# Kernel optimization log

Measured on AMD Instinct MI355X. Metric: run time of the kernel, lower is better.

Reference implementation:

```python
import jax, jax.numpy as jnp
import numpy as np
from functools import partial

B = 8192
BS = 6           # board_size
NSQ = BS * BS    # 36
FLAT = 128 * NSQ # 4608
EPS = 1e-5


def _conv(x, w, b):
    # x: (N,C,H,W), w: (O,I,3,3), SAME padding
    y = jax.lax.conv_general_dilated(x, w, (1, 1), 'SAME',
                                     dimension_numbers=('NCHW', 'OIHW', 'NCHW'))
    return y + b[None, :, None, None]


def _bn_eval(x, g, b, m, v):
    inv = jax.lax.rsqrt(v + EPS)
    return (x - m[None, :, None, None]) * (g * inv)[None, :, None, None] + b[None, :, None, None]


def _ln(x, g, b):
    mu = jnp.mean(x, axis=-1, keepdims=True)
    var = jnp.mean(jnp.square(x - mu), axis=-1, keepdims=True)
    return (x - mu) * jax.lax.rsqrt(var + EPS) * g + b


def _lin(x, w, b):
    return x @ w.T + b


def setup_inputs() -> dict:
    key = jax.random.key(0)
    ks = iter(jax.random.split(key, 64))
    nrm = lambda shape, s=0.05: jax.random.normal(next(ks), shape, jnp.float32) * s
    d = {}
    d['x'] = jax.random.normal(next(ks), (B, 4, BS, BS), jnp.float32)
    d['conv1_w'] = nrm((64, 4, 3, 3)); d['conv1_b'] = nrm((64,))
    d['bn1_g'] = jnp.ones((64,)); d['bn1_b'] = jnp.zeros((64,))
    d['bn1_m'] = nrm((64,)); d['bn1_v'] = jnp.ones((64,))
    d['conv2_w'] = nrm((128, 64, 3, 3)); d['conv2_b'] = nrm((128,))
    d['bn2_g'] = jnp.ones((128,)); d['bn2_b'] = jnp.zeros((128,))
    d['bn2_m'] = nrm((128,)); d['bn2_v'] = jnp.ones((128,))
    d['conv3_w'] = nrm((128, 128, 3, 3)); d['conv3_b'] = nrm((128,))
    d['bn3_g'] = jnp.ones((128,)); d['bn3_b'] = jnp.zeros((128,))
    d['bn3_m'] = nrm((128,)); d['bn3_v'] = jnp.ones((128,))
    d['pfc1_w'] = nrm((256, FLAT)); d['pfc1_b'] = nrm((256,))
    d['pln_g'] = jnp.ones((256,)); d['pln_b'] = jnp.zeros((256,))
    d['pfc2_w'] = nrm((NSQ, 256)); d['pfc2_b'] = nrm((NSQ,))
    d['mfc1_w'] = nrm((256, FLAT + NSQ)); d['mfc1_b'] = nrm((256,))
    d['mln_g'] = jnp.ones((256,)); d['mln_b'] = jnp.zeros((256,))
    d['mfc2_w'] = nrm((NSQ, 256)); d['mfc2_b'] = nrm((NSQ,))
    d['vfc1_w'] = nrm((256, FLAT)); d['vfc1_b'] = nrm((256,))
    d['vln_g'] = jnp.ones((256,)); d['vln_b'] = jnp.zeros((256,))
    d['vfc2_w'] = nrm((1, 256)); d['vfc2_b'] = nrm((1,))
    return d


def reference(x, conv1_w, conv1_b, bn1_g, bn1_b, bn1_m, bn1_v,
              conv2_w, conv2_b, bn2_g, bn2_b, bn2_m, bn2_v,
              conv3_w, conv3_b, bn3_g, bn3_b, bn3_m, bn3_v,
              pfc1_w, pfc1_b, pln_g, pln_b, pfc2_w, pfc2_b,
              mfc1_w, mfc1_b, mln_g, mln_b, mfc2_w, mfc2_b,
              vfc1_w, vfc1_b, vln_g, vln_b, vfc2_w, vfc2_b):
    h = jax.nn.relu(_bn_eval(_conv(x, conv1_w, conv1_b), bn1_g, bn1_b, bn1_m, bn1_v))
    h = jax.nn.relu(_bn_eval(_conv(h, conv2_w, conv2_b), bn2_g, bn2_b, bn2_m, bn2_v))
    h = jax.nn.relu(_bn_eval(_conv(h, conv3_w, conv3_b), bn3_g, bn3_b, bn3_m, bn3_v))
    feats = h.reshape(-1, FLAT)  # (B, 4608)

    piece_h = jax.nn.relu(_ln(_lin(feats, pfc1_w, pfc1_b), pln_g, pln_b))
    piece_logits = _lin(piece_h, pfc2_w, pfc2_b)  # (B, 36)

    # eval-mode: one-hot of argmax piece
    sel = jax.nn.one_hot(jnp.argmax(piece_logits, axis=1), NSQ, dtype=feats.dtype)
    move_in = jnp.concatenate([feats, sel], axis=1)  # (B, 4644)
    move_h = jax.nn.relu(_ln(_lin(move_in, mfc1_w, mfc1_b), mln_g, mln_b))
    move_logits = _lin(move_h, mfc2_w, mfc2_b)  # (B, 36)

    val_h = jax.nn.relu(_ln(_lin(feats, vfc1_w, vfc1_b), vln_g, vln_b))
    val = _lin(val_h, vfc2_w, vfc2_b)  # (B, 1)

    piece_adv = piece_logits - jnp.mean(piece_logits, axis=1, keepdims=True)
    move_adv = move_logits - jnp.mean(move_logits, axis=1, keepdims=True)

    # action_idx = i*36 + j  ->  fused outer-sum broadcast, reshape to (B, 1296)
    q = val[:, :, None] + piece_adv[:, :, None] + move_adv[:, None, :]
    return q.reshape(-1, NSQ * NSQ)
```

## Files before the change

kernel.cpp:

```cpp
#include <hip/hip_runtime.h>
#include <hip/hip_bf16.h>

#define BQ 8192
#define CHUNK 2048
#define NCHUNK 4
typedef __attribute__((ext_vector_type(8))) __bf16 bf16x8;
typedef __attribute__((ext_vector_type(4))) float f32x4;
typedef __attribute__((ext_vector_type(4))) int int4v;

__device__ __forceinline__ f32x4 mfma16(bf16x8 a, bf16x8 b, f32x4 c) {
    return __builtin_amdgcn_mfma_f32_16x16x32_bf16(a, b, c, 0, 0, 0);
}

__device__ __forceinline__ void split3(float v, __hip_bfloat16& s0,
                                       __hip_bfloat16& s1, __hip_bfloat16& s2) {
    s0 = __float2bfloat16(v);
    float r = v - __bfloat162float(s0);
    s1 = __float2bfloat16(r);
    r -= __bfloat162float(s1);
    s2 = __float2bfloat16(r);
}

__device__ __forceinline__ int pair_a(int pp) { return (0x211000 >> (4 * pp)) & 0xF; }
__device__ __forceinline__ int pair_w(int pp) { return (0x010210 >> (4 * pp)) & 0xF; }


__global__ void prep_scalars_k(
    const float* __restrict__ c1b, const float* __restrict__ g1,
    const float* __restrict__ b1,  const float* __restrict__ m1,
    const float* __restrict__ v1,
    const float* __restrict__ c2b, const float* __restrict__ g2,
    const float* __restrict__ b2,  const float* __restrict__ m2,
    const float* __restrict__ v2,
    const float* __restrict__ c3b, const float* __restrict__ g3,
    const float* __restrict__ b3,  const float* __restrict__ m3,
    const float* __restrict__ v3,
    const float* __restrict__ pfb, const float* __restrict__ vfb,
    const float* __restrict__ mfb,
    float* __restrict__ scale1, float* __restrict__ bias1f,
    float* __restrict__ scale2, float* __restrict__ bias2f,
    float* __restrict__ scale3, float* __restrict__ bias3f,
    float* __restrict__ biasfc)
{
    int t = threadIdx.x;
    if (t < 64) {
        float s = g1[t] * rsqrtf(v1[t] + 1e-5f);
        scale1[t] = s;
        bias1f[t] = (c1b[t] - m1[t]) * s + b1[t];
    }
    if (t < 128) {
        float s2 = g2[t] * rsqrtf(v2[t] + 1e-5f);
        scale2[t] = s2;
        bias2f[t] = (c2b[t] - m2[t]) * s2 + b2[t];
        float s3 = g3[t] * rsqrtf(v3[t] + 1e-5f);
        scale3[t] = s3;
        bias3f[t] = (c3b[t] - m3[t]) * s3 + b3[t];
    }
    if (t < 256)      biasfc[t] = pfb[t];
    else if (t < 512) biasfc[t] = vfb[t - 256];
    else              biasfc[t] = mfb[t - 512];
}

template<int CIN>
__global__ void prep_convw_k(const float* __restrict__ w,
                             __hip_bfloat16* __restrict__ wt, size_t planeW)
{
    int id = blockIdx.x * 256 + threadIdx.x;
    int kk = id & 31;
    int n  = (id >> 5) & 127;
    int kt = id >> 12;
    int k  = kt * 32 + kk;
    int s  = k / CIN;
    int i  = k & (CIN - 1);
    __hip_bfloat16 s0, s1, s2;
    split3(w[(n * CIN + i) * 9 + s], s0, s1, s2);
    size_t dest = (size_t)kt * 4096 + ((n >> 5) * 1024) + (((n >> 4) & 1) * 512)
                + ((kk >> 3) * 128) + ((n & 15) * 8) + (kk & 7);
    wt[dest] = s0; wt[dest + planeW] = s1; wt[dest + 2 * planeW] = s2;
}

__global__ void prep_bigw_k(const float* __restrict__ pw,
                            const float* __restrict__ vw,
                            const float* __restrict__ mw,
                            __hip_bfloat16* __restrict__ bigw, size_t planeBW)
{
    int id = blockIdx.x * 256 + threadIdx.x;
    int kk = id & 31;
    int n  = (id >> 5) % 768;
    int kt = id / (32 * 768);
    int k2 = kt * 32 + kk;
    int c  = k2 & 127, p = k2 >> 7;
    int k  = c * 36 + p;
    float v;
    if (n < 256)      v = pw[n * 4608 + k];
    else if (n < 512) v = vw[(n - 256) * 4608 + k];
    else              v = mw[(n - 512) * 4644 + k];
    __hip_bfloat16 s0, s1, s2;
    split3(v, s0, s1, s2);
    size_t dest = (size_t)kt * 24576 + ((n >> 7) * 4096) + (((n >> 6) & 1) * 2048)
                + (((n >> 4) & 3) * 512) + ((kk >> 3) * 128) + ((n & 15) * 8) + (kk & 7);
    bigw[dest] = s0; bigw[dest + planeBW] = s1; bigw[dest + 2 * planeBW] = s2;
}

__global__ void prep_selw_k(const float* __restrict__ mw,
                            float* __restrict__ selw)
{
    int j = blockIdx.x, d = threadIdx.x;
    selw[j * 256 + d] = mw[d * 4644 + 4608 + j];
}


__global__ __launch_bounds__(256)
void conv1_k(const float* __restrict__ x,
             const float* __restrict__ w,
             const float* __restrict__ scale, const float* __restrict__ biasf,
             __hip_bfloat16* __restrict__ out, size_t planeA,
             int b_base)
{
    __shared__ float wl[64 * 37];
    int tid = threadIdx.x;
    for (int c = tid; c < 64 * 36; c += 256) {
        int o = c / 36, k = c - o * 36;
        wl[o * 37 + k] = w[c];
    }
    __syncthreads();
    unsigned gid = blockIdx.x * 256 + tid;
    int o = gid & 63;
    unsigned bp = gid >> 6;
    unsigned b = bp / 36;
    int p = bp - b * 36;
    int py = p / 6, px = p - py * 6;
    const float* xb = x + (size_t)(b_base + b) * 4 * 36;
    float acc = 0.f;
#pragma unroll
    for (int i = 0; i < 4; ++i) {
#pragma unroll
        for (int s = 0; s < 9; ++s) {
            int ny = py + s / 3 - 1, nx = px + s % 3 - 1;
            if ((unsigned)ny < 6u && (unsigned)nx < 6u)
                acc += xb[i * 36 + ny * 6 + nx] * wl[o * 37 + i * 9 + s];
        }
    }
    float v = fmaxf(acc * scale[o] + biasf[o], 0.f);
    __hip_bfloat16 s0, s1, s2;
    split3(v, s0, s1, s2);
    size_t idx = (size_t)bp * 64 + o;
    out[idx] = s0; out[idx + planeA] = s1; out[idx + 2 * planeA] = s2;
}

template<int CIN>
__global__ __launch_bounds__(256, 4)
void conv_gemm_k(const __hip_bfloat16* __restrict__ in, size_t planeA,
                 const __hip_bfloat16* __restrict__ wt, size_t planeW,
                 const float* __restrict__ scale,
                 const float* __restrict__ biasf,
                 __hip_bfloat16* __restrict__ out, size_t planeO)
{
    constexpr int PS  = CIN + 8;
    constexpr int CPB = CIN / 32;
    constexpr int NSLICE = CPB * 9;
    constexpr int XS_ELEMS = 72 * PS;
    __shared__ __align__(16) __hip_bfloat16 smem[XS_ELEMS + CIN];
    __hip_bfloat16* xs = smem;

    const int tid  = threadIdx.x;
    const int wave = tid >> 6, lane = tid & 63;
    const int m16  = lane & 15, quad = lane >> 4;
    const int b0   = blockIdx.x * 2;

    if (tid < CIN) smem[XS_ELEMS + tid] = __float2bfloat16(0.f);

    f32x4 acc[5][2];
#pragma unroll
    for (int i = 0; i < 5; ++i) { acc[i][0] = f32x4{0,0,0,0}; acc[i][1] = f32x4{0,0,0,0}; }

    const int bo0 = wave * 1024 + lane * 8;
    const int bo1 = bo0 + 512;

    constexpr int CHPP = CIN / 8;
    for (int pp = 0; pp < 6; ++pp) {
        const __hip_bfloat16* inb = in + (size_t)pair_a(pp) * planeA + (size_t)b0 * 36 * CIN;
        const __hip_bfloat16* wP  = wt + (size_t)pair_w(pp) * planeW;
        const bool stage_x = (pp == 0) || (pair_a(pp) != pair_a(pp - 1));

        if (stage_x) {
            __syncthreads();
            for (int c = tid; c < 72 * CHPP; c += 256) {
                int pix = c / CHPP;
                int off = (c - pix * CHPP) * 8;
                *(int4v*)(xs + pix * PS + off) = *(const int4v*)(inb + pix * CIN + off);
            }
            __syncthreads();
        }

        bf16x8 wc0 = *(const bf16x8*)(wP + bo0);
        bf16x8 wc1 = *(const bf16x8*)(wP + bo1);

        for (int s = 0; s < 9; ++s) {
            const int dy = s / 3 - 1, dx = s % 3 - 1;
            int aoff[5];
#pragma unroll
            for (int rt = 0; rt < 5; ++rt) {
                int m   = rt * 16 + m16;
                int img = m >= 36;
                int p   = m - img * 36;
                int py  = p / 6, px = p - py * 6;
                int ny  = py + dy, nx = px + dx;
                bool ok = (m < 72) && ((unsigned)ny < 6u) && ((unsigned)nx < 6u);
                int base = ok ? ((img * 36 + ny * 6 + nx) * PS) : XS_ELEMS;
                aoff[rt] = base + quad * 8;
            }
#pragma unroll
            for (int c = 0; c < CPB; ++c) {
                const int kt = s * CPB + c;
                const int ktn = (kt + 1 < NSLICE) ? (kt + 1) : 0;
                const __hip_bfloat16* wN = wP + (size_t)ktn * 4096;
                bf16x8 wn0 = *(const bf16x8*)(wN + bo0);
                bf16x8 wn1 = *(const bf16x8*)(wN + bo1);
                const int coff = c * 32;
#pragma unroll
                for (int rt = 0; rt < 5; ++rt) {
                    bf16x8 af = *(const bf16x8*)(smem + aoff[rt] + coff);
                    acc[rt][0] = mfma16(af, wc0, acc[rt][0]);
                    acc[rt][1] = mfma16(af, wc1, acc[rt][1]);
                }
                wc0 = wn0; wc1 = wn1;
            }
        }
    }

#pragma unroll
    for (int ct = 0; ct < 2; ++ct) {
        const int n = wave * 32 + ct * 16 + m16;
        const float sc = scale[n], bi = biasf[n];
#pragma unroll
        for (int rt = 0; rt < 5; ++rt) {
            const int mrow = rt * 16 + quad * 4;
            if (mrow < 72) {
#pragma unroll
                for (int r = 0; r < 4; ++r) {
                    float v = fmaxf(acc[rt][ct][r] * sc + bi, 0.f);
                    __hip_bfloat16 s0, s1, s2;
                    split3(v, s0, s1, s2);
                    size_t idx = (size_t)(b0 * 36 + mrow + r) * 128 + n;
                    out[idx] = s0; out[idx + planeO] = s1; out[idx + 2 * planeO] = s2;
                }
            }
        }
    }
}


template<int NW, int NKT>
__device__ __forceinline__ void fc_body(
    const __hip_bfloat16* __restrict__ Ap,
    const __hip_bfloat16* __restrict__ Bp,
    size_t planeBW, int kt0,
    float* __restrict__ outp, size_t m0,
    __hip_bfloat16* smem, int tid, int wave, int lane)
{
    constexpr int ABUF = 4096;
    constexpr int NPH = NW * NKT;
    const int m16 = lane & 15, quad = lane >> 4;
    const int wr = wave >> 1, wc = wave & 1;
    const int cr = tid >> 2, co = (tid & 3) * 8;

    f32x4 acc[4][4];
#pragma unroll
    for (int i = 0; i < 4; ++i)
#pragma unroll
        for (int j = 0; j < 4; ++j) acc[i][j] = f32x4{0,0,0,0};

    int ao[4];
#pragma unroll
    for (int i = 0; i < 4; ++i) ao[i] = wr * 2048 + i * 512 + lane * 8;
    const int bofs = wc * 2048 + lane * 8;
    const int adst = ((cr >> 4) & 3) * 512 + (tid & 3) * 128 + (cr & 15) * 8;

    auto ldA = [&](int ktr, int4v& a0, int4v& a1) {
        const __hip_bfloat16* base = Ap + (m0 + cr) * 4608 + (kt0 + ktr) * 32 + co;
        a0 = *(const int4v*)base;
        a1 = *(const int4v*)(base + (size_t)64 * 4608);
    };
    auto ldB = [&](int p, bf16x8* bf) {
        const int ktr = p / NW, w = p - ktr * NW;
        const __hip_bfloat16* base = Bp + (size_t)w * planeBW
                                   + (size_t)(kt0 + ktr) * 24576 + bofs;
#pragma unroll
        for (int i = 0; i < 4; ++i) bf[i] = *(const bf16x8*)(base + i * 512);
    };
    auto stA = [&](int buf, int4v a0, int4v a1) {
        __hip_bfloat16* base = smem + buf * ABUF;
        *(int4v*)(base + adst) = a0;
        *(int4v*)(base + 2048 + adst) = a1;
    };

    int4v pa0, pa1, qa0, qa1;
    bf16x8 Bc[4], B1[4], Bn[4];
    {
        int4v a0, a1;
        ldA(0, a0, a1);
        ldB(0, Bc);
        ldA(1, pa0, pa1);
        if (NPH > 1) ldB(1, B1);
        stA(0, a0, a1);
    }
    __syncthreads();
    int cur = 0;

    for (int ktr = 0; ktr < NKT; ++ktr) {
        { int ktn = (ktr + 2 < NKT) ? (ktr + 2) : 0; ldA(ktn, qa0, qa1); }
        const __hip_bfloat16* base = smem + cur * ABUF;
        bf16x8 af[4];
#pragma unroll
        for (int i = 0; i < 4; ++i) af[i] = *(const bf16x8*)(base + ao[i]);
#pragma unroll
        for (int w = 0; w < NW; ++w) {
            int p2 = ktr * NW + w + 2;
            if (p2 >= NPH) p2 = 0;
            ldB(p2, Bn);
#pragma unroll
            for (int i = 0; i < 4; ++i)
#pragma unroll
                for (int j = 0; j < 4; ++j)
                    acc[i][j] = mfma16(af[i], Bc[j], acc[i][j]);
#pragma unroll
            for (int i = 0; i < 4; ++i) { Bc[i] = B1[i]; B1[i] = Bn[i]; }
        }
        if (ktr + 1 < NKT) stA(cur ^ 1, pa0, pa1);
        __syncthreads();
        cur ^= 1;
        pa0 = qa0; pa1 = qa1;
    }

#pragma unroll
    for (int i = 0; i < 4; ++i) {
        const int row = wr * 64 + i * 16 + quad * 4;
#pragma unroll
        for (int j = 0; j < 4; ++j) {
            const int col = wc * 64 + j * 16 + m16;
#pragma unroll
            for (int r = 0; r < 4; ++r)
                outp[(m0 + row + r) * 768 + col] = acc[i][j][r];
        }
    }
}

__global__ __launch_bounds__(256, 3)
void fc_partial_k(const __hip_bfloat16* __restrict__ A, size_t planeF,
                  const __hip_bfloat16* __restrict__ Bw, size_t planeBW,
                  float* __restrict__ partial)
{
    constexpr int ABUF = 4096;
    __shared__ __align__(16) __hip_bfloat16 smem[2 * ABUF];
    const int tid = threadIdx.x, wave = tid >> 6, lane = tid & 63;
    const int mblk = blockIdx.x & 15;
    int rest = blockIdx.x >> 4;
    const int nblk = rest % 6;
    const int slot = rest / 6;
    const size_t m0 = (size_t)mblk * 128;

    const __hip_bfloat16* Bp = Bw + (size_t)nblk * 4096;
    float* outp = partial + (size_t)slot * CHUNK * 768 + (size_t)nblk * 128;

    if (slot < 6) {
        fc_body<3, 24>(A, Bp, planeBW, slot * 24, outp, m0, smem, tid, wave, lane);
    } else if (slot < 10) {
        fc_body<2, 36>(A + planeF, Bp, planeBW, (slot - 6) * 36, outp, m0, smem, tid, wave, lane);
    } else {
        fc_body<1, 72>(A + 2 * planeF, Bp, planeBW, (slot - 10) * 72, outp, m0, smem, tid, wave, lane);
    }
}


__global__ __launch_bounds__(256)
void heads_k(const float* __restrict__ partial,
             const float* __restrict__ biasfc,
             const float* __restrict__ pln_g, const float* __restrict__ pln_b,
             const float* __restrict__ pfc2_w, const float* __restrict__ pfc2_b,
             const float* __restrict__ mln_g, const float* __restrict__ mln_b,
             const float* __restrict__ mfc2_w, const float* __restrict__ mfc2_b,
             const float* __restrict__ vln_g, const float* __restrict__ vln_b,
             const float* __restrict__ vfc2_w, const float* __restrict__ vfc2_b,
             const float* __restrict__ selw,
             float* __restrict__ q,
             int b_base)
{
    __shared__ float hp[256], hv[256], hm[256];
    __shared__ float pl[36], ml[36];
    __shared__ float red[4];
    __shared__ float valv, plm_s, mlm_s;
    __shared__ int amax_s;

    const int tid = threadIdx.x, wave = tid >> 6, lane = tid & 63;
    const size_t b = blockIdx.x;
    const size_t bg = b_base + b;

    float pp = biasfc[tid], vv = biasfc[256 + tid], mm = biasfc[512 + tid];
#pragma unroll
    for (int k = 0; k < 12; ++k) {
        const float* row = partial + (size_t)k * CHUNK * 768 + b * 768;
        pp += row[tid]; vv += row[256 + tid]; mm += row[512 + tid];
    }

    auto warpSum = [&](float v) {
        v += __shfl_xor(v, 1);  v += __shfl_xor(v, 2);  v += __shfl_xor(v, 4);
        v += __shfl_xor(v, 8);  v += __shfl_xor(v, 16); v += __shfl_xor(v, 32);
        return v;
    };
    auto blockSum = [&](float v) {
        v = warpSum(v);
        if (lane == 0) red[wave] = v;
        __syncthreads();
        float s = red[0] + red[1] + red[2] + red[3];
        __syncthreads();
        return s;
    };
    auto lnrelu = [&](float x, const float* g, const float* bb) {
        float mu  = blockSum(x) * (1.f / 256.f);
        float d   = x - mu;
        float var = blockSum(d * d) * (1.f / 256.f);
        float y   = d * rsqrtf(var + 1e-5f) * g[tid] + bb[tid];
        return fmaxf(y, 0.f);
    };

    hp[tid] = lnrelu(pp, pln_g, pln_b);
    hv[tid] = lnrelu(vv, vln_g, vln_b);
    __syncthreads();

    {
        float h0 = hp[lane], h1 = hp[64 + lane], h2 = hp[128 + lane], h3 = hp[192 + lane];
#pragma unroll
        for (int jj = 0; jj < 9; ++jj) {
            int j = wave * 9 + jj;
            const float* wr_ = pfc2_w + j * 256;
            float s = h0 * wr_[lane] + h1 * wr_[64 + lane]
                    + h2 * wr_[128 + lane] + h3 * wr_[192 + lane];
            s = warpSum(s);
            if (lane == 0) pl[j] = s + pfc2_b[j];
        }
        if (wave == 0) {
            float g0 = hv[lane], g1 = hv[64 + lane], g2 = hv[128 + lane], g3 = hv[192 + lane];
            float s = g0 * vfc2_w[lane] + g1 * vfc2_w[64 + lane]
                    + g2 * vfc2_w[128 + lane] + g3 * vfc2_w[192 + lane];
            s = warpSum(s);
            if (lane == 0) valv = s + vfc2_b[0];
        }
    }
    __syncthreads();
    if (tid == 0) {
        float m = -1e30f, s = 0.f; int idx = 0;
        for (int j = 0; j < 36; ++j) { float v = pl[j]; s += v; if (v > m) { m = v; idx = j; } }
        plm_s = s * (1.f / 36.f); amax_s = idx;
    }
    __syncthreads();

    mm += selw[amax_s * 256 + tid];
    hm[tid] = lnrelu(mm, mln_g, mln_b);
    __syncthreads();
    {
        float h0 = hm[lane], h1 = hm[64 + lane], h2 = hm[128 + lane], h3 = hm[192 + lane];
#pragma unroll
        for (int jj = 0; jj < 9; ++jj) {
            int j = wave * 9 + jj;
            const float* wr_ = mfc2_w + j * 256;
            float s = h0 * wr_[lane] + h1 * wr_[64 + lane]
                    + h2 * wr_[128 + lane] + h3 * wr_[192 + lane];
            s = warpSum(s);
            if (lane == 0) ml[j] = s + mfc2_b[j];
        }
    }
    __syncthreads();
    if (tid == 0) {
        float s = 0.f;
        for (int j = 0; j < 36; ++j) s += ml[j];
        mlm_s = s * (1.f / 36.f);
    }
    __syncthreads();

    const float val = valv, plm = plm_s, mlm = mlm_s;
    for (int idx = tid; idx < 1296; idx += 256) {
        int i = idx / 36, j = idx - i * 36;
        q[bg * 1296 + idx] = val + (pl[i] - plm) + (ml[j] - mlm);
    }
}


extern "C" void kernel_launch(void* const* d_in, const int* in_sizes, int n_in,
                              void* d_out, int out_size, void* d_ws, size_t ws_size,
                              hipStream_t stream)
{
    const float* x       = (const float*)d_in[0];
    const float* conv1_w = (const float*)d_in[1];
    const float* conv1_b = (const float*)d_in[2];
    const float* bn1_g   = (const float*)d_in[3];
    const float* bn1_b   = (const float*)d_in[4];
    const float* bn1_m   = (const float*)d_in[5];
    const float* bn1_v   = (const float*)d_in[6];
    const float* conv2_w = (const float*)d_in[7];
    const float* conv2_b = (const float*)d_in[8];
    const float* bn2_g   = (const float*)d_in[9];
    const float* bn2_b   = (const float*)d_in[10];
    const float* bn2_m   = (const float*)d_in[11];
    const float* bn2_v   = (const float*)d_in[12];
    const float* conv3_w = (const float*)d_in[13];
    const float* conv3_b = (const float*)d_in[14];
    const float* bn3_g   = (const float*)d_in[15];
    const float* bn3_b   = (const float*)d_in[16];
    const float* bn3_m   = (const float*)d_in[17];
    const float* bn3_v   = (const float*)d_in[18];
    const float* pfc1_w  = (const float*)d_in[19];
    const float* pfc1_b  = (const float*)d_in[20];
    const float* pln_g   = (const float*)d_in[21];
    const float* pln_b   = (const float*)d_in[22];
    const float* pfc2_w  = (const float*)d_in[23];
    const float* pfc2_b  = (const float*)d_in[24];
    const float* mfc1_w  = (const float*)d_in[25];
    const float* mfc1_b  = (const float*)d_in[26];
    const float* mln_g   = (const float*)d_in[27];
    const float* mln_b   = (const float*)d_in[28];
    const float* mfc2_w  = (const float*)d_in[29];
    const float* mfc2_b  = (const float*)d_in[30];
    const float* vfc1_w  = (const float*)d_in[31];
    const float* vfc1_b  = (const float*)d_in[32];
    const float* vln_g   = (const float*)d_in[33];
    const float* vln_b   = (const float*)d_in[34];
    const float* vfc2_w  = (const float*)d_in[35];
    const float* vfc2_b  = (const float*)d_in[36];

    const size_t planeW2 = 576 * 128;
    const size_t planeW3 = 1152 * 128;
    const size_t planeBW = (size_t)4608 * 768;
    const size_t planeA1 = (size_t)CHUNK * 36 * 64;
    const size_t planeA2 = (size_t)CHUNK * 36 * 128;

    char* ws = (char*)d_ws;
    size_t off = 0;
    auto alloc = [&](size_t bytes) -> char* {
        char* p = ws + off; off += (bytes + 255) & ~(size_t)255; return p;
    };
    __hip_bfloat16* w2t  = (__hip_bfloat16*)alloc(3 * planeW2 * 2);
    __hip_bfloat16* w3t  = (__hip_bfloat16*)alloc(3 * planeW3 * 2);
    __hip_bfloat16* bigw = (__hip_bfloat16*)alloc(3 * planeBW * 2);
    float* selw   = (float*)alloc(36 * 256 * 4);
    float* scale1 = (float*)alloc(64 * 4);
    float* bias1f = (float*)alloc(64 * 4);
    float* scale2 = (float*)alloc(128 * 4);
    float* bias2f = (float*)alloc(128 * 4);
    float* scale3 = (float*)alloc(128 * 4);
    float* bias3f = (float*)alloc(128 * 4);
    float* biasfc = (float*)alloc(768 * 4);
    char* A1 = alloc(3 * planeA2 * 2);
    char* A2 = alloc((size_t)12 * CHUNK * 768 * 4);

    prep_scalars_k<<<1, 768, 0, stream>>>(
        conv1_b, bn1_g, bn1_b, bn1_m, bn1_v,
        conv2_b, bn2_g, bn2_b, bn2_m, bn2_v,
        conv3_b, bn3_g, bn3_b, bn3_m, bn3_v,
        pfc1_b, vfc1_b, mfc1_b,
        scale1, bias1f, scale2, bias2f, scale3, bias3f, biasfc);
    prep_convw_k<64><<<288, 256, 0, stream>>>(conv2_w, w2t, planeW2);
    prep_convw_k<128><<<576, 256, 0, stream>>>(conv3_w, w3t, planeW3);
    prep_bigw_k<<<13824, 256, 0, stream>>>(pfc1_w, vfc1_w, mfc1_w, bigw, planeBW);
    prep_selw_k<<<36, 256, 0, stream>>>(mfc1_w, selw);

    __hip_bfloat16* h1s  = (__hip_bfloat16*)A1;
    __hip_bfloat16* h2s  = (__hip_bfloat16*)A2;
    __hip_bfloat16* h3s  = (__hip_bfloat16*)A1;
    float*          fpar = (float*)A2;

    for (int cchunk = 0; cchunk < NCHUNK; ++cchunk) {
        const int b_base = cchunk * CHUNK;
        conv1_k<<<CHUNK * 36 * 64 / 256, 256, 0, stream>>>(
            x, conv1_w, scale1, bias1f, h1s, planeA1, b_base);
        conv_gemm_k<64><<<CHUNK / 2, 256, 0, stream>>>(
            h1s, planeA1, w2t, planeW2, scale2, bias2f, h2s, planeA2);
        conv_gemm_k<128><<<CHUNK / 2, 256, 0, stream>>>(
            h2s, planeA2, w3t, planeW3, scale3, bias3f, h3s, planeA2);
        fc_partial_k<<<1152, 256, 0, stream>>>(h3s, planeA2, bigw, planeBW, fpar);
        heads_k<<<CHUNK, 256, 0, stream>>>(fpar, biasfc,
            pln_g, pln_b, pfc2_w, pfc2_b,
            mln_g, mln_b, mfc2_w, mfc2_b,
            vln_g, vln_b, vfc2_w, vfc2_b,
            selw, (float*)d_out, b_base);
    }
}
```

Baseline: 1.698 ms.

## Use larger batch chunks with fewer split-K slots when workspace allows

When the workspace is large enough, the kernel processes the batch in chunks of 4096 instead of 2048 and splits the FC reduction into 6 slots instead of 12. Each FC block then runs a longer K loop, and the heads kernel sums fewer partials. This cuts launch count and partial-sum traffic. In exchange the FC loop trip count becomes a runtime value with unroll 2, which may cost some scheduling quality. The conv kernels also get more blocks per launch, and the path taken depends on ws_size at runtime.

```diff
diff --git a/kernel.cpp b/kernel.cpp
--- a/kernel.cpp
+++ b/kernel.cpp
@@ -2,8 +2,6 @@
 #include <hip/hip_bf16.h>
 
 #define BQ 8192
-#define CHUNK 2048
-#define NCHUNK 4
 typedef __attribute__((ext_vector_type(8))) __bf16 bf16x8;
 typedef __attribute__((ext_vector_type(4))) float f32x4;
 typedef __attribute__((ext_vector_type(4))) int int4v;
@@ -251,16 +249,16 @@
 }
 
 
-template<int NW, int NKT>
+template<int NW>
 __device__ __forceinline__ void fc_body(
     const __hip_bfloat16* __restrict__ Ap,
     const __hip_bfloat16* __restrict__ Bp,
-    size_t planeBW, int kt0,
+    size_t planeBW, int kt0, int NKT,
     float* __restrict__ outp, size_t m0,
     __hip_bfloat16* smem, int tid, int wave, int lane)
 {
     constexpr int ABUF = 4096;
-    constexpr int NPH = NW * NKT;
+    const int NPH = NW * NKT;
     const int m16 = lane & 15, quad = lane >> 4;
     const int wr = wave >> 1, wc = wave & 1;
     const int cr = tid >> 2, co = (tid & 3) * 8;
@@ -308,6 +306,7 @@
     __syncthreads();
     int cur = 0;
 
+#pragma unroll 2
     for (int ktr = 0; ktr < NKT; ++ktr) {
         { int ktn = (ktr + 2 < NKT) ? (ktr + 2) : 0; ldA(ktn, qa0, qa1); }
         const __hip_bfloat16* base = smem + cur * ABUF;
@@ -349,26 +348,36 @@
 __global__ __launch_bounds__(256, 3)
 void fc_partial_k(const __hip_bfloat16* __restrict__ A, size_t planeF,
                   const __hip_bfloat16* __restrict__ Bw, size_t planeBW,
-                  float* __restrict__ partial)
+                  float* __restrict__ partial,
+                  int chunk, int big)
 {
     constexpr int ABUF = 4096;
     __shared__ __align__(16) __hip_bfloat16 smem[2 * ABUF];
     const int tid = threadIdx.x, wave = tid >> 6, lane = tid & 63;
-    const int mblk = blockIdx.x & 15;
-    int rest = blockIdx.x >> 4;
+    const int nmblk = chunk >> 7;
+    const int mblk = blockIdx.x & (nmblk - 1);
+    int rest = blockIdx.x / nmblk;
     const int nblk = rest % 6;
     const int slot = rest / 6;
     const size_t m0 = (size_t)mblk * 128;
 
     const __hip_bfloat16* Bp = Bw + (size_t)nblk * 4096;
-    float* outp = partial + (size_t)slot * CHUNK * 768 + (size_t)nblk * 128;
-
-    if (slot < 6) {
-        fc_body<3, 24>(A, Bp, planeBW, slot * 24, outp, m0, smem, tid, wave, lane);
-    } else if (slot < 10) {
-        fc_body<2, 36>(A + planeF, Bp, planeBW, (slot - 6) * 36, outp, m0, smem, tid, wave, lane);
+    float* outp = partial + (size_t)slot * chunk * 768 + (size_t)nblk * 128;
+
+    if (big) {
+        if (slot < 3)
+            fc_body<3>(A, Bp, planeBW, slot * 48, 48, outp, m0, smem, tid, wave, lane);
+        else if (slot < 5)
+            fc_body<2>(A + planeF, Bp, planeBW, (slot - 3) * 72, 72, outp, m0, smem, tid, wave, lane);
+        else
+            fc_body<1>(A + 2 * planeF, Bp, planeBW, 0, 144, outp, m0, smem, tid, wave, lane);
     } else {
-        fc_body<1, 72>(A + 2 * planeF, Bp, planeBW, (slot - 10) * 72, outp, m0, smem, tid, wave, lane);
+        if (slot < 6)
+            fc_body<3>(A, Bp, planeBW, slot * 24, 24, outp, m0, smem, tid, wave, lane);
+        else if (slot < 10)
+            fc_body<2>(A + planeF, Bp, planeBW, (slot - 6) * 36, 36, outp, m0, smem, tid, wave, lane);
+        else
+            fc_body<1>(A + 2 * planeF, Bp, planeBW, (slot - 10) * 72, 72, outp, m0, smem, tid, wave, lane);
     }
 }
 
@@ -384,7 +393,7 @@
              const float* __restrict__ vfc2_w, const float* __restrict__ vfc2_b,
              const float* __restrict__ selw,
              float* __restrict__ q,
-             int b_base)
+             int b_base, int ns, int chunk)
 {
     __shared__ float hp[256], hv[256], hm[256];
     __shared__ float pl[36], ml[36];
@@ -397,9 +406,8 @@
     const size_t bg = b_base + b;
 
     float pp = biasfc[tid], vv = biasfc[256 + tid], mm = biasfc[512 + tid];
-#pragma unroll
-    for (int k = 0; k < 12; ++k) {
-        const float* row = partial + (size_t)k * CHUNK * 768 + b * 768;
+    for (int k = 0; k < ns; ++k) {
+        const float* row = partial + (size_t)k * chunk * 768 + b * 768;
         pp += row[tid]; vv += row[256 + tid]; mm += row[512 + tid];
     }
 
@@ -531,8 +539,28 @@
     const size_t planeW2 = 576 * 128;
     const size_t planeW3 = 1152 * 128;
     const size_t planeBW = (size_t)4608 * 768;
-    const size_t planeA1 = (size_t)CHUNK * 36 * 64;
-    const size_t planeA2 = (size_t)CHUNK * 36 * 128;
+
+    auto layout_total = [&](int CH, int NS) -> size_t {
+        size_t t = 0;
+        auto add = [&](size_t b) { t += (b + 255) & ~(size_t)255; };
+        add(3 * planeW2 * 2); add(3 * planeW3 * 2); add(3 * planeBW * 2);
+        add(36 * 256 * 4);
+        add(64 * 4); add(64 * 4); add(128 * 4); add(128 * 4);
+        add(128 * 4); add(128 * 4); add(768 * 4);
+        size_t pA2 = (size_t)CH * 36 * 128;
+        add(3 * pA2 * 2);
+        size_t par = (size_t)NS * CH * 768 * 4;
+        add((3 * pA2 * 2 > par) ? 3 * pA2 * 2 : par);
+        return t;
+    };
+
+    const int big = (layout_total(4096, 6) <= ws_size) ? 1 : 0;
+    const int CH  = big ? 4096 : 2048;
+    const int NS  = big ? 6 : 12;
+    const int NCH = BQ / CH;
+
+    const size_t planeA1 = (size_t)CH * 36 * 64;
+    const size_t planeA2 = (size_t)CH * 36 * 128;
 
     char* ws = (char*)d_ws;
     size_t off = 0;
@@ -550,8 +578,9 @@
     float* scale3 = (float*)alloc(128 * 4);
     float* bias3f = (float*)alloc(128 * 4);
     float* biasfc = (float*)alloc(768 * 4);
+    size_t parBytes = (size_t)NS * CH * 768 * 4;
     char* A1 = alloc(3 * planeA2 * 2);
-    char* A2 = alloc((size_t)12 * CHUNK * 768 * 4);
+    char* A2 = alloc((3 * planeA2 * 2 > parBytes) ? 3 * planeA2 * 2 : parBytes);
 
     prep_scalars_k<<<1, 768, 0, stream>>>(
         conv1_b, bn1_g, bn1_b, bn1_m, bn1_v,
@@ -569,19 +598,20 @@
     __hip_bfloat16* h3s  = (__hip_bfloat16*)A1;
     float*          fpar = (float*)A2;
 
-    for (int cchunk = 0; cchunk < NCHUNK; ++cchunk) {
-        const int b_base = cchunk * CHUNK;
-        conv1_k<<<CHUNK * 36 * 64 / 256, 256, 0, stream>>>(
+    for (int cchunk = 0; cchunk < NCH; ++cchunk) {
+        const int b_base = cchunk * CH;
+        conv1_k<<<CH * 9, 256, 0, stream>>>(
             x, conv1_w, scale1, bias1f, h1s, planeA1, b_base);
-        conv_gemm_k<64><<<CHUNK / 2, 256, 0, stream>>>(
+        conv_gemm_k<64><<<CH / 2, 256, 0, stream>>>(
             h1s, planeA1, w2t, planeW2, scale2, bias2f, h2s, planeA2);
-        conv_gemm_k<128><<<CHUNK / 2, 256, 0, stream>>>(
+        conv_gemm_k<128><<<CH / 2, 256, 0, stream>>>(
             h2s, planeA2, w3t, planeW3, scale3, bias3f, h3s, planeA2);
-        fc_partial_k<<<1152, 256, 0, stream>>>(h3s, planeA2, bigw, planeBW, fpar);
-        heads_k<<<CHUNK, 256, 0, stream>>>(fpar, biasfc,
+        fc_partial_k<<<(CH / 128) * 6 * NS / (big ? 2 : 1) * (big ? 2 : 1), 256, 0, stream>>>(
+            h3s, planeA2, bigw, planeBW, fpar, CH, big);
+        heads_k<<<CH, 256, 0, stream>>>(fpar, biasfc,
             pln_g, pln_b, pfc2_w, pfc2_b,
             mln_g, mln_b, mfc2_w, mfc2_b,
             vln_g, vln_b, vfc2_w, vfc2_b,
-            selw, (float*)d_out, b_base);
-    }
-}
+            selw, (float*)d_out, b_base, NS, CH);
+    }
+}
```

Result: faster. 1.603 ms (-5.6%).
